# Optimization experiments

Measured on AMD Instinct MI355X. Metric: run time of the kernel, lower is better.

## Reference

```python
import jax, jax.numpy as jnp
import numpy as np

N = 100_000   # nodes
E = 1_600_000 # edges (avg degree 16)
D0, D1, D2 = 128, 64, 64


def _linp(key, n_out, n_in):
    kw, kb = jax.random.split(key)
    s = 1.0 / np.sqrt(n_in)
    W = jax.random.uniform(kw, (n_out, n_in), jnp.float32, -s, s)
    b = jax.random.uniform(kb, (n_out,), jnp.float32, -s, s)
    return W, b


def setup_inputs() -> dict:
    key = jax.random.key(0)
    ks = jax.random.split(key, 9)
    h = jax.random.normal(ks[0], (N, D0), jnp.float32)
    # guarantee every row has at least one edge (avoids empty-row softmax / 0-std NaNs)
    rows = jnp.concatenate([jnp.arange(N, dtype=jnp.int32),
                            jax.random.randint(ks[1], (E - N,), 0, N, jnp.int32)])
    cols = jax.random.randint(ks[2], (E,), 0, N, jnp.int32)
    edge_index = jnp.stack([rows, cols])  # [2, E], row = softmax segment
    W11, b11 = _linp(ks[3], D1, D0)
    W12, b12 = _linp(ks[4], 1, D1)
    W13, b13 = _linp(ks[5], D1, D0)
    W21, b21 = _linp(ks[6], D2, D1)
    W22, b22 = _linp(ks[7], 1, D2)
    W23, b23 = _linp(ks[8], D2, D1)
    return dict(h=h, edge_index=edge_index,
                W11=W11, b11=b11, W12=W12, b12=b12, W13=W13, b13=b13,
                W21=W21, b21=b21, W22=W22, b22=b22, W23=W23, b23=b23)


def reference(h, edge_index, W11, b11, W12, b12, W13, b13,
              W21, b21, W22, b22, W23, b23):
    src, dst = edge_index[0], edge_index[1]

    def gat_layer(x, Wa, ba, We, be, Wv, bv):
        a = jnp.tanh(x @ Wa.T + ba)                       # [N, d] node scores (l11/l21)
        e = jnp.tanh((a[src] + a[dst]) @ We.T + be)[:, 0] # [E] per-edge logit (l12/l22)
        # per-row (segment) softmax over src = row index
        m = jax.ops.segment_max(e, src, num_segments=N)
        ex = jnp.exp(e - m[src])
        denom = jax.ops.segment_sum(ex, src, num_segments=N)
        att = ex / denom[src]                             # [E]
        v = jnp.tanh(x @ Wv.T + bv)                       # [N, d] values (l13/l23)
        out = jax.ops.segment_sum(att[:, None] * v[dst], src, num_segments=N)  # sparse mm
        return out / jnp.std(out, -1, keepdims=True, ddof=1)  # torch.std is unbiased

    h = gat_layer(h, W11, b11, W12, b12, W13, b13)
    h = gat_layer(h, W21, b21, W22, b22, W23, b23)
    return h
```

## Files before the change

kernel.cpp:

```cpp
#include <hip/hip_runtime.h>


#define WS_ALIGN 256
#define BIN_SHIFT 7
#define BIN_NODES 128
#define BIN_CAP 2560
#define MAX_BINS 1024
#define EPB 4096
#define AGGR_BLOCKS 1563

typedef __attribute__((ext_vector_type(8))) short short8;
typedef __attribute__((ext_vector_type(4))) short short4_t;
typedef __attribute__((ext_vector_type(4))) float f32x4;

__device__ __forceinline__ float fast_tanh(float x) {
  x = fminf(15.f, fmaxf(-15.f, x));
  float e = __expf(2.f * x);
  return (e - 1.f) * __builtin_amdgcn_rcpf(e + 1.f);
}

__device__ __forceinline__ unsigned short f32_to_bf16_rne(float f) {
  unsigned u = __float_as_uint(f);
  unsigned r = u + 0x7fffu + ((u >> 16) & 1u);
  return (unsigned short)(r >> 16);
}

__device__ __forceinline__ void prepw_one(const float* __restrict__ Wa,
                                          const float* __restrict__ Wv,
                                          short* __restrict__ Wh, short* __restrict__ Wl,
                                          int K, int i) {
  int KBLK = K / 32;
  int j = i & 7;
  int c = (i >> 3) & 15;
  int q = (i >> 7) & 3;
  int r = i >> 9;
  int nt = r / KBLK, kb = r - nt * KBLK;
  int row = nt * 16 + c;
  int col = kb * 32 + q * 8 + j;
  float f = (row < 64) ? Wa[row * K + col] : Wv[(row - 64) * K + col];
  unsigned u = __float_as_uint(f);
  float hf = __uint_as_float(u & 0xffff0000u);
  Wh[i] = (short)(u >> 16);
  Wl[i] = (short)(__float_as_uint(f - hf) >> 16);
}

__global__ void k_setup(const float* __restrict__ W11, const float* __restrict__ W13,
                        short* __restrict__ Wh1, short* __restrict__ Wl1,
                        const float* __restrict__ W21, const float* __restrict__ W23,
                        short* __restrict__ Wh2, short* __restrict__ Wl2,
                        int* __restrict__ cursor, int nb) {
  int i = blockIdx.x * 256 + threadIdx.x;
  if (i < 16384) {
    prepw_one(W11, W13, Wh1, Wl1, 128, i);
  } else if (i < 16384 + 8192) {
    prepw_one(W21, W23, Wh2, Wl2, 64, i - 16384);
  } else {
    int b = i - 24576;
    if (b < nb) cursor[b] = b * BIN_CAP;
  }
}

__global__ __launch_bounds__(256) void k_bin(const int* __restrict__ src,
                                             const int* __restrict__ dst,
                                             int* __restrict__ cursor,
                                             int* __restrict__ binned, int E, int nb) {
  __shared__ int ssrc[EPB];
  __shared__ int sdst[EPB];
  __shared__ int hist[MAX_BINS];
  __shared__ int base[MAX_BINS];
  int t = threadIdx.x;
  for (int i = t; i < nb; i += 256) hist[i] = 0;
  __syncthreads();
  int e0 = blockIdx.x * EPB;
  for (int i = t; i < EPB; i += 256) {
    int e = e0 + i;
    int sv = -1, dv = 0;
    if (e < E) {
      sv = src[e];
      dv = dst[e];
      atomicAdd(&hist[sv >> BIN_SHIFT], 1);
    }
    ssrc[i] = sv;
    sdst[i] = dv;
  }
  __syncthreads();
  for (int b = t; b < nb; b += 256) {
    int c = hist[b];
    base[b] = c ? atomicAdd(&cursor[b], c) : 0;
    hist[b] = 0;
  }
  __syncthreads();
  for (int i = t; i < EPB; i += 256) {
    int sv = ssrc[i];
    if (sv >= 0) {
      int b = sv >> BIN_SHIFT;
      int r = atomicAdd(&hist[b], 1);
      int pos = base[b] + r;
      if (pos < (b + 1) * BIN_CAP)
        binned[pos] = (sdst[i] << BIN_SHIFT) | (sv & (BIN_NODES - 1));
    }
  }
}

__global__ __launch_bounds__(256) void k_sort_bin(int* __restrict__ binned,
                                                  const int* __restrict__ cursor,
                                                  int* __restrict__ rs,
                                                  int* __restrict__ re, int n) {
  __shared__ int ents[BIN_CAP];
  __shared__ int sorted[BIN_CAP];
  __shared__ int hist[BIN_NODES];
  __shared__ int scan[BIN_NODES];
  __shared__ int cur[BIN_NODES];
  int bin = blockIdx.x;
  int t = threadIdx.x;
  int nbase = bin << BIN_SHIFT;
  int cnt = cursor[bin] - bin * BIN_CAP;
  if (cnt > BIN_CAP) cnt = BIN_CAP;
  if (t < BIN_NODES) hist[t] = 0;
  __syncthreads();
  int* bp = binned + (size_t)bin * BIN_CAP;
  for (int i = t; i < cnt; i += 256) {
    int pk = bp[i];
    ents[i] = pk;
    atomicAdd(&hist[pk & (BIN_NODES - 1)], 1);
  }
  __syncthreads();
  if (t < BIN_NODES) scan[t] = hist[t];
  __syncthreads();
  for (int off = 1; off < BIN_NODES; off <<= 1) {
    int add = (t < BIN_NODES && t >= off) ? scan[t - off] : 0;
    __syncthreads();
    if (t < BIN_NODES) scan[t] += add;
    __syncthreads();
  }
  if (t < BIN_NODES) {
    int ex = scan[t] - hist[t];
    cur[t] = ex;
    int node = nbase + t;
    if (node < n) {
      rs[node] = bin * BIN_CAP + ex;
      re[node] = bin * BIN_CAP + ex + hist[t];
    }
  }
  __syncthreads();
  for (int i = t; i < cnt; i += 256) {
    int pk = ents[i];
    int pos = atomicAdd(&cur[pk & (BIN_NODES - 1)], 1);
    sorted[pos] = pk;
  }
  __syncthreads();
  for (int i = t; i < cnt; i += 256) {
    int pk = sorted[i];
    int node = pk & (BIN_NODES - 1);
    int hi = scan[node];
    int lo = hi - hist[node];
    int r = lo;
    for (int j = lo; j < hi; j++) {
      int pj = sorted[j];
      r += (pj < pk) || (pj == pk && j < i);
    }
    ents[r] = pk >> BIN_SHIFT;
  }
  __syncthreads();
  for (int i = t; i < cnt; i += 256) bp[i] = ents[i];
}

template <int K>
__global__ __launch_bounds__(256) void k_node(
    const float* __restrict__ x, const short* __restrict__ Wh,
    const short* __restrict__ Wl, const float* __restrict__ ba,
    const float* __restrict__ we, const float* __restrict__ bv,
    unsigned short* __restrict__ v_out, float* __restrict__ s_out, int n) {
  constexpr int KBLK = K / 32;
  constexpr int RS = K + 8;
  __shared__ short sah[64 * RS];
  __shared__ short sal[64 * RS];
  __shared__ float sP[2][64];
  int t = threadIdx.x;
  int l = t & 63;
  int w = t >> 6;
  int q = l >> 4, c = l & 15;
  int node0b = blockIdx.x * 64;

  {
    const float4* xg = (const float4*)(x + (size_t)node0b * K);
    constexpr int R4 = K / 4;
#pragma unroll
    for (int it = 0; it < 64 * R4 / 256; it++) {
      int i = it * 256 + t;
      int r = i / R4, k4 = i - r * R4;
      float4 val = (node0b + r < n) ? xg[i] : (float4){0.f, 0.f, 0.f, 0.f};
      float xv[4] = {val.x, val.y, val.z, val.w};
      short4_t hi, lo;
#pragma unroll
      for (int j = 0; j < 4; j++) {
        unsigned u = __float_as_uint(xv[j]);
        hi[j] = (short)(u >> 16);
        float hf = __uint_as_float(u & 0xffff0000u);
        lo[j] = (short)(__float_as_uint(xv[j] - hf) >> 16);
      }
      *(short4_t*)&sah[r * RS + k4 * 4] = hi;
      *(short4_t*)&sal[r * RS + k4 * 4] = lo;
    }
  }

  const short8* WhF = (const short8*)Wh;
  const short8* WlF = (const short8*)Wl;
  short8 wfh[2][KBLK], wfl[2][KBLK];
#pragma unroll
  for (int mt = 0; mt < 2; mt++)
#pragma unroll
    for (int kb = 0; kb < KBLK; kb++) {
      size_t f = (size_t)((2 * w + mt) * KBLK + kb) * 64 + l;
      wfh[mt][kb] = WhF[f];
      wfl[mt][kb] = WlF[f];
    }
  __syncthreads();

  f32x4 acc[4][2];
#pragma unroll
  for (int ns = 0; ns < 4; ns++)
#pragma unroll
    for (int mt = 0; mt < 2; mt++) acc[ns][mt] = (f32x4){0.f, 0.f, 0.f, 0.f};

#pragma unroll
  for (int ns = 0; ns < 4; ns++) {
#pragma unroll
    for (int kb = 0; kb < KBLK; kb++) {
      int off = (ns * 16 + c) * RS + kb * 32 + q * 8;
      short8 ah = *(const short8*)&sah[off];
      short8 al = *(const short8*)&sal[off];
#pragma unroll
      for (int mt = 0; mt < 2; mt++) {
        acc[ns][mt] = __builtin_amdgcn_mfma_f32_16x16x32_bf16(ah, wfh[mt][kb], acc[ns][mt], 0, 0, 0);
        acc[ns][mt] = __builtin_amdgcn_mfma_f32_16x16x32_bf16(ah, wfl[mt][kb], acc[ns][mt], 0, 0, 0);
        acc[ns][mt] = __builtin_amdgcn_mfma_f32_16x16x32_bf16(al, wfh[mt][kb], acc[ns][mt], 0, 0, 0);
      }
    }
  }

  if (w < 2) {
    float bav0 = ba[w * 32 + c], wev0 = we[w * 32 + c];
    float bav1 = ba[w * 32 + 16 + c], wev1 = we[w * 32 + 16 + c];
#pragma unroll
    for (int ns = 0; ns < 4; ns++) {
#pragma unroll
      for (int r = 0; r < 4; r++) {
        float pv = fast_tanh(acc[ns][0][r] + bav0) * wev0 +
                   fast_tanh(acc[ns][1][r] + bav1) * wev1;
#pragma unroll
        for (int mm = 1; mm < 16; mm <<= 1) pv += __shfl_xor(pv, mm, 64);
        if (c == 0) sP[w][ns * 16 + q * 4 + r] = pv;
      }
    }
  } else {
    int wv = w - 2;
    float bvv0 = bv[wv * 32 + c], bvv1 = bv[wv * 32 + 16 + c];
#pragma unroll
    for (int ns = 0; ns < 4; ns++) {
#pragma unroll
      for (int r = 0; r < 4; r++) {
        int node = node0b + ns * 16 + q * 4 + r;
        if (node < n) {
          v_out[(size_t)node * 64 + wv * 32 + c] =
              f32_to_bf16_rne(fast_tanh(acc[ns][0][r] + bvv0));
          v_out[(size_t)node * 64 + wv * 32 + 16 + c] =
              f32_to_bf16_rne(fast_tanh(acc[ns][1][r] + bvv1));
        }
      }
    }
  }
  __syncthreads();
  if (t < 64) {
    int node = node0b + t;
    if (node < n) s_out[node] = sP[0][t] + sP[1][t];
  }
}

__global__ __launch_bounds__(256) void k_aggr(const int* __restrict__ rs,
                                              const int* __restrict__ re,
                                              const int* __restrict__ col,
                                              const float* __restrict__ s,
                                              const float* __restrict__ be_p,
                                              const unsigned short* __restrict__ v,
                                              float* __restrict__ out, int n) {
  int wid = (int)((blockIdx.x * 256 + threadIdx.x) >> 6);
  int nwv = (int)gridDim.x * 4;
  int l = threadIdx.x & 63;
  int q = l >> 4;
  int g = l & 15;
  int qb = l & 48;
  float be = be_p[0];
  int ngroups = (n + 3) >> 2;
  if (wid >= ngroups) return;

  int pnode = wid * 4 + q;
  bool pvn = pnode < n;
  int pe0 = pvn ? rs[pnode] : 0;
  int pe1 = pvn ? re[pnode] : 0;
  float psrow = pvn ? s[pnode] : 0.f;
  int pc;
  float psc;
  {
    int prem = pe1 - pe0;
    pc = (g < prem) ? col[pe0 + g] : 0;
    psc = (g < prem) ? s[pc] : 0.f;
  }

  for (int grp = wid; grp < ngroups; grp += nwv) {
    int e0 = pe0, e1 = pe1;
    float srow = psrow;
    int c0 = pc;
    float sc0 = psc;
    int nxt = grp + nwv;
    if (nxt < ngroups) {
      int nn = nxt * 4 + q;
      bool nv = nn < n;
      pe0 = nv ? rs[nn] : 0;
      pe1 = nv ? re[nn] : 0;
      psrow = nv ? s[nn] : 0.f;
    }
    int m = e1 - e0;
    float a0 = 0.f, a1 = 0.f, a2 = 0.f, a3 = 0.f;
    float dl = 0.f;

    {
      float w = (g < m) ? __expf(fast_tanh(srow + sc0 + be)) : 0.f;
      dl += w;
#pragma unroll
      for (int jj = 0; jj < 16; jj++) {
        int cj = __shfl(c0, qb + jj, 64);
        float wj = __shfl(w, qb + jj, 64);
        uint2 pk = *(const uint2*)(v + ((size_t)cj << 6) + (g << 2));
        a0 = fmaf(wj, __uint_as_float(pk.x << 16), a0);
        a1 = fmaf(wj, __uint_as_float(pk.x & 0xffff0000u), a1);
        a2 = fmaf(wj, __uint_as_float(pk.y << 16), a2);
        a3 = fmaf(wj, __uint_as_float(pk.y & 0xffff0000u), a3);
      }
    }
    if (nxt < ngroups) {
      int nrem = pe1 - pe0;
      pc = (g < nrem) ? col[pe0 + g] : 0;
      psc = (g < nrem) ? s[pc] : 0.f;
    }
    for (int cb = 16; !__all(m - cb <= 0); cb += 16) {
      bool act = (cb + g) < m;
      int c = act ? col[e0 + cb + g] : 0;
      float w = act ? __expf(fast_tanh(srow + s[c] + be)) : 0.f;
      dl += w;
#pragma unroll
      for (int jj = 0; jj < 16; jj++) {
        int cj = __shfl(c, qb + jj, 64);
        float wj = __shfl(w, qb + jj, 64);
        uint2 pk = *(const uint2*)(v + ((size_t)cj << 6) + (g << 2));
        a0 = fmaf(wj, __uint_as_float(pk.x << 16), a0);
        a1 = fmaf(wj, __uint_as_float(pk.x & 0xffff0000u), a1);
        a2 = fmaf(wj, __uint_as_float(pk.y << 16), a2);
        a3 = fmaf(wj, __uint_as_float(pk.y & 0xffff0000u), a3);
      }
    }

#pragma unroll
    for (int mm = 1; mm < 16; mm <<= 1) dl += __shfl_xor(dl, mm, 64);
    float inv = __builtin_amdgcn_rcpf(dl);
    float o0 = a0 * inv, o1 = a1 * inv, o2 = a2 * inv, o3 = a3 * inv;
    float t0 = o0 + o1 + o2 + o3;
    float t1 = o0 * o0 + o1 * o1 + o2 * o2 + o3 * o3;
#pragma unroll
    for (int mm = 1; mm < 16; mm <<= 1) {
      t0 += __shfl_xor(t0, mm, 64);
      t1 += __shfl_xor(t1, mm, 64);
    }
    float var = (t1 - t0 * t0 * (1.0f / 64.f)) * (1.0f / 63.f);
    float isd = __builtin_amdgcn_rsqf(var);
    int cnode = grp * 4 + q;
    if (cnode < n) {
      float4 r = {o0 * isd, o1 * isd, o2 * isd, o3 * isd};
      *(float4*)&out[(size_t)cnode * 64 + (g << 2)] = r;
    }
  }
}

extern "C" void kernel_launch(void* const* d_in, const int* in_sizes, int n_in,
                              void* d_out, int out_size, void* d_ws, size_t ws_size,
                              hipStream_t stream) {
  const float* h = (const float*)d_in[0];
  const int* ei = (const int*)d_in[1];
  const float* W11 = (const float*)d_in[2];
  const float* b11 = (const float*)d_in[3];
  const float* W12 = (const float*)d_in[4];
  const float* b12 = (const float*)d_in[5];
  const float* W13 = (const float*)d_in[6];
  const float* b13 = (const float*)d_in[7];
  const float* W21 = (const float*)d_in[8];
  const float* b21 = (const float*)d_in[9];
  const float* W22 = (const float*)d_in[10];
  const float* b22 = (const float*)d_in[11];
  const float* W23 = (const float*)d_in[12];
  const float* b23 = (const float*)d_in[13];

  const int N = in_sizes[0] / 128;
  const int E = in_sizes[1] / 2;
  const int* src = ei;
  const int* dst = ei + E;
  const int NB = (N + BIN_NODES - 1) >> BIN_SHIFT;

  char* p = (char*)d_ws;
  auto alloc = [&](size_t bytes) -> void* {
    void* r = (void*)p;
    p += (bytes + WS_ALIGN - 1) / WS_ALIGN * WS_ALIGN;
    return r;
  };
  int* cursor = (int*)alloc((size_t)NB * 4);
  int* binned = (int*)alloc((size_t)NB * BIN_CAP * 4);
  int* rsb = (int*)alloc((size_t)N * 4);
  int* reb = (int*)alloc((size_t)N * 4);
  float* sbuf = (float*)alloc((size_t)N * 4);
  unsigned short* vbuf = (unsigned short*)alloc((size_t)N * 64 * 2);
  float* out1 = (float*)alloc((size_t)N * 64 * 4);
  short* Wh1 = (short*)alloc(128 * 128 * 2);
  short* Wl1 = (short*)alloc(128 * 128 * 2);
  short* Wh2 = (short*)alloc(128 * 64 * 2);
  short* Wl2 = (short*)alloc(128 * 64 * 2);

  k_setup<<<(24576 + NB + 255) / 256, 256, 0, stream>>>(
      W11, W13, Wh1, Wl1, W21, W23, Wh2, Wl2, cursor, NB);

  k_bin<<<(E + EPB - 1) / EPB, 256, 0, stream>>>(src, dst, cursor, binned, E, NB);
  k_sort_bin<<<NB, 256, 0, stream>>>(binned, cursor, rsb, reb, N);

  k_node<128><<<(N + 63) / 64, 256, 0, stream>>>(h, Wh1, Wl1, b11, W12, b13, vbuf, sbuf, N);
  k_aggr<<<AGGR_BLOCKS, 256, 0, stream>>>(rsb, reb, binned, sbuf, b12, vbuf, out1, N);

  k_node<64><<<(N + 63) / 64, 256, 0, stream>>>(out1, Wh2, Wl2, b21, W22, b23, vbuf, sbuf, N);
  k_aggr<<<AGGR_BLOCKS, 256, 0, stream>>>(rsb, reb, binned, sbuf, b22, vbuf, (float*)d_out, N);
}
```

Before: 281.6 us.

## Merge setup into binning and run bin sort alongside first node transform

Weight bf16 splitting now runs as extra blocks of the binning kernel, and the cursor init becomes a memset with counts made relative to each bin. The per-bin sort and the first-layer node GEMM are combined into one launch, with blocks choosing their role by block index and sharing a common shared-memory buffer. This cuts kernel launches and lets the independent sort and GEMM work overlap on the device. Aggregation grid size also rises from 1563 to 2048 blocks. The combined kernel reserves the larger of the two shared-memory footprints for every block, which may lower occupancy for the sort blocks.

```diff
diff --git a/kernel.cpp b/kernel.cpp
--- a/kernel.cpp
+++ b/kernel.cpp
@@ -7,7 +7,7 @@
 #define BIN_CAP 2560
 #define MAX_BINS 1024
 #define EPB 4096
-#define AGGR_BLOCKS 1563
+#define AGGR_BLOCKS 2048
 
 typedef __attribute__((ext_vector_type(8))) short short8;
 typedef __attribute__((ext_vector_type(4))) short short4_t;
@@ -44,34 +44,30 @@
   Wl[i] = (short)(__float_as_uint(f - hf) >> 16);
 }
 
-__global__ void k_setup(const float* __restrict__ W11, const float* __restrict__ W13,
-                        short* __restrict__ Wh1, short* __restrict__ Wl1,
-                        const float* __restrict__ W21, const float* __restrict__ W23,
-                        short* __restrict__ Wh2, short* __restrict__ Wl2,
-                        int* __restrict__ cursor, int nb) {
-  int i = blockIdx.x * 256 + threadIdx.x;
-  if (i < 16384) {
-    prepw_one(W11, W13, Wh1, Wl1, 128, i);
-  } else if (i < 16384 + 8192) {
-    prepw_one(W21, W23, Wh2, Wl2, 64, i - 16384);
-  } else {
-    int b = i - 24576;
-    if (b < nb) cursor[b] = b * BIN_CAP;
-  }
-}
-
-__global__ __launch_bounds__(256) void k_bin(const int* __restrict__ src,
-                                             const int* __restrict__ dst,
-                                             int* __restrict__ cursor,
-                                             int* __restrict__ binned, int E, int nb) {
+__global__ __launch_bounds__(256) void k_bin_setup(
+    const int* __restrict__ src, const int* __restrict__ dst,
+    int* __restrict__ cnt0, int* __restrict__ binned, int E, int nb, int binBlks,
+    const float* __restrict__ W11, const float* __restrict__ W13,
+    short* __restrict__ Wh1, short* __restrict__ Wl1,
+    const float* __restrict__ W21, const float* __restrict__ W23,
+    short* __restrict__ Wh2, short* __restrict__ Wl2) {
   __shared__ int ssrc[EPB];
   __shared__ int sdst[EPB];
   __shared__ int hist[MAX_BINS];
   __shared__ int base[MAX_BINS];
   int t = threadIdx.x;
+  if ((int)blockIdx.x >= binBlks) {
+    int i = ((int)blockIdx.x - binBlks) * 256 + t;
+    if (i < 16384) {
+      prepw_one(W11, W13, Wh1, Wl1, 128, i);
+    } else if (i < 24576) {
+      prepw_one(W21, W23, Wh2, Wl2, 64, i - 16384);
+    }
+    return;
+  }
   for (int i = t; i < nb; i += 256) hist[i] = 0;
   __syncthreads();
-  int e0 = blockIdx.x * EPB;
+  int e0 = (int)blockIdx.x * EPB;
   for (int i = t; i < EPB; i += 256) {
     int e = e0 + i;
     int sv = -1, dv = 0;
@@ -86,7 +82,7 @@
   __syncthreads();
   for (int b = t; b < nb; b += 256) {
     int c = hist[b];
-    base[b] = c ? atomicAdd(&cursor[b], c) : 0;
+    base[b] = c ? (b * BIN_CAP + atomicAdd(&cnt0[b], c)) : 0;
     hist[b] = 0;
   }
   __syncthreads();
@@ -102,19 +98,124 @@
   }
 }
 
-__global__ __launch_bounds__(256) void k_sort_bin(int* __restrict__ binned,
-                                                  const int* __restrict__ cursor,
-                                                  int* __restrict__ rs,
-                                                  int* __restrict__ re, int n) {
-  __shared__ int ents[BIN_CAP];
-  __shared__ int sorted[BIN_CAP];
-  __shared__ int hist[BIN_NODES];
-  __shared__ int scan[BIN_NODES];
-  __shared__ int cur[BIN_NODES];
-  int bin = blockIdx.x;
+template <int K>
+__device__ __forceinline__ void node_body(
+    short* __restrict__ sah, short* __restrict__ sal, float* __restrict__ sP,
+    int bid, const float* __restrict__ x, const short* __restrict__ Wh,
+    const short* __restrict__ Wl, const float* __restrict__ ba,
+    const float* __restrict__ we, const float* __restrict__ bv,
+    unsigned short* __restrict__ v_out, float* __restrict__ s_out, int n) {
+  constexpr int KBLK = K / 32;
+  constexpr int RS = K + 8;
+  int t = threadIdx.x;
+  int l = t & 63;
+  int w = t >> 6;
+  int q = l >> 4, c = l & 15;
+  int node0b = bid * 64;
+
+  {
+    const float4* xg = (const float4*)(x + (size_t)node0b * K);
+    constexpr int R4 = K / 4;
+#pragma unroll
+    for (int it = 0; it < 64 * R4 / 256; it++) {
+      int i = it * 256 + t;
+      int r = i / R4, k4 = i - r * R4;
+      float4 val = (node0b + r < n) ? xg[i] : (float4){0.f, 0.f, 0.f, 0.f};
+      float xv[4] = {val.x, val.y, val.z, val.w};
+      short4_t hi, lo;
+#pragma unroll
+      for (int j = 0; j < 4; j++) {
+        unsigned u = __float_as_uint(xv[j]);
+        hi[j] = (short)(u >> 16);
+        float hf = __uint_as_float(u & 0xffff0000u);
+        lo[j] = (short)(__float_as_uint(xv[j] - hf) >> 16);
+      }
+      *(short4_t*)&sah[r * RS + k4 * 4] = hi;
+      *(short4_t*)&sal[r * RS + k4 * 4] = lo;
+    }
+  }
+
+  const short8* WhF = (const short8*)Wh;
+  const short8* WlF = (const short8*)Wl;
+  short8 wfh[2][KBLK], wfl[2][KBLK];
+#pragma unroll
+  for (int mt = 0; mt < 2; mt++)
+#pragma unroll
+    for (int kb = 0; kb < KBLK; kb++) {
+      size_t f = (size_t)((2 * w + mt) * KBLK + kb) * 64 + l;
+      wfh[mt][kb] = WhF[f];
+      wfl[mt][kb] = WlF[f];
+    }
+  __syncthreads();
+
+  f32x4 acc[4][2];
+#pragma unroll
+  for (int ns = 0; ns < 4; ns++)
+#pragma unroll
+    for (int mt = 0; mt < 2; mt++) acc[ns][mt] = (f32x4){0.f, 0.f, 0.f, 0.f};
+
+#pragma unroll
+  for (int ns = 0; ns < 4; ns++) {
+#pragma unroll
+    for (int kb = 0; kb < KBLK; kb++) {
+      int off = (ns * 16 + c) * RS + kb * 32 + q * 8;
+      short8 ah = *(const short8*)&sah[off];
+      short8 al = *(const short8*)&sal[off];
+#pragma unroll
+      for (int mt = 0; mt < 2; mt++) {
+        acc[ns][mt] = __builtin_amdgcn_mfma_f32_16x16x32_bf16(ah, wfh[mt][kb], acc[ns][mt], 0, 0, 0);
+        acc[ns][mt] = __builtin_amdgcn_mfma_f32_16x16x32_bf16(ah, wfl[mt][kb], acc[ns][mt], 0, 0, 0);
+        acc[ns][mt] = __builtin_amdgcn_mfma_f32_16x16x32_bf16(al, wfh[mt][kb], acc[ns][mt], 0, 0, 0);
+      }
+    }
+  }
+
+  if (w < 2) {
+    float bav0 = ba[w * 32 + c], wev0 = we[w * 32 + c];
+    float bav1 = ba[w * 32 + 16 + c], wev1 = we[w * 32 + 16 + c];
+#pragma unroll
+    for (int ns = 0; ns < 4; ns++) {
+#pragma unroll
+      for (int r = 0; r < 4; r++) {
+        float pv = fast_tanh(acc[ns][0][r] + bav0) * wev0 +
+                   fast_tanh(acc[ns][1][r] + bav1) * wev1;
+#pragma unroll
+        for (int mm = 1; mm < 16; mm <<= 1) pv += __shfl_xor(pv, mm, 64);
+        if (c == 0) sP[w * 64 + ns * 16 + q * 4 + r] = pv;
+      }
+    }
+  } else {
+    int wv = w - 2;
+    float bvv0 = bv[wv * 32 + c], bvv1 = bv[wv * 32 + 16 + c];
+#pragma unroll
+    for (int ns = 0; ns < 4; ns++) {
+#pragma unroll
+      for (int r = 0; r < 4; r++) {
+        int node = node0b + ns * 16 + q * 4 + r;
+        if (node < n) {
+          v_out[(size_t)node * 64 + wv * 32 + c] =
+              f32_to_bf16_rne(fast_tanh(acc[ns][0][r] + bvv0));
+          v_out[(size_t)node * 64 + wv * 32 + 16 + c] =
+              f32_to_bf16_rne(fast_tanh(acc[ns][1][r] + bvv1));
+        }
+      }
+    }
+  }
+  __syncthreads();
+  if (t < 64) {
+    int node = node0b + t;
+    if (node < n) s_out[node] = sP[t] + sP[64 + t];
+  }
+}
+
+__device__ __forceinline__ void sort_body(
+    int* __restrict__ ents, int* __restrict__ sorted, int* __restrict__ hist,
+    int* __restrict__ scan, int* __restrict__ cur, int bin,
+    int* __restrict__ binned, const int* __restrict__ cnt0,
+    int* __restrict__ rs, int* __restrict__ re, int n) {
   int t = threadIdx.x;
   int nbase = bin << BIN_SHIFT;
-  int cnt = cursor[bin] - bin * BIN_CAP;
+  int cnt = cnt0[bin];
   if (cnt > BIN_CAP) cnt = BIN_CAP;
   if (t < BIN_NODES) hist[t] = 0;
   __syncthreads();
@@ -165,116 +266,43 @@
   for (int i = t; i < cnt; i += 256) bp[i] = ents[i];
 }
 
+__global__ __launch_bounds__(256) void k_node128_sort(
+    int nodeBlks,
+    const float* __restrict__ x, const short* __restrict__ Wh,
+    const short* __restrict__ Wl, const float* __restrict__ ba,
+    const float* __restrict__ we, const float* __restrict__ bv,
+    unsigned short* __restrict__ v_out, float* __restrict__ s_out, int n,
+    int* __restrict__ binned, const int* __restrict__ cnt0,
+    int* __restrict__ rs, int* __restrict__ re) {
+  __shared__ __align__(16) char smem[64 * 136 * 4 + 512];
+  if ((int)blockIdx.x < nodeBlks) {
+    short* sah = (short*)smem;
+    short* sal = (short*)(smem + 64 * 136 * 2);
+    float* sP = (float*)(smem + 64 * 136 * 4);
+    node_body<128>(sah, sal, sP, (int)blockIdx.x, x, Wh, Wl, ba, we, bv,
+                   v_out, s_out, n);
+  } else {
+    int* ents = (int*)smem;
+    int* sorted = ents + BIN_CAP;
+    int* hist = sorted + BIN_CAP;
+    int* scan = hist + BIN_NODES;
+    int* cur = scan + BIN_NODES;
+    sort_body(ents, sorted, hist, scan, cur, (int)blockIdx.x - nodeBlks,
+              binned, cnt0, rs, re, n);
+  }
+}
+
 template <int K>
 __global__ __launch_bounds__(256) void k_node(
     const float* __restrict__ x, const short* __restrict__ Wh,
     const short* __restrict__ Wl, const float* __restrict__ ba,
     const float* __restrict__ we, const float* __restrict__ bv,
     unsigned short* __restrict__ v_out, float* __restrict__ s_out, int n) {
-  constexpr int KBLK = K / 32;
-  constexpr int RS = K + 8;
-  __shared__ short sah[64 * RS];
-  __shared__ short sal[64 * RS];
-  __shared__ float sP[2][64];
-  int t = threadIdx.x;
-  int l = t & 63;
-  int w = t >> 6;
-  int q = l >> 4, c = l & 15;
-  int node0b = blockIdx.x * 64;
-
-  {
-    const float4* xg = (const float4*)(x + (size_t)node0b * K);
-    constexpr int R4 = K / 4;
-#pragma unroll
-    for (int it = 0; it < 64 * R4 / 256; it++) {
-      int i = it * 256 + t;
-      int r = i / R4, k4 = i - r * R4;
-      float4 val = (node0b + r < n) ? xg[i] : (float4){0.f, 0.f, 0.f, 0.f};
-      float xv[4] = {val.x, val.y, val.z, val.w};
-      short4_t hi, lo;
-#pragma unroll
-      for (int j = 0; j < 4; j++) {
-        unsigned u = __float_as_uint(xv[j]);
-        hi[j] = (short)(u >> 16);
-        float hf = __uint_as_float(u & 0xffff0000u);
-        lo[j] = (short)(__float_as_uint(xv[j] - hf) >> 16);
-      }
-      *(short4_t*)&sah[r * RS + k4 * 4] = hi;
-      *(short4_t*)&sal[r * RS + k4 * 4] = lo;
-    }
-  }
-
-  const short8* WhF = (const short8*)Wh;
-  const short8* WlF = (const short8*)Wl;
-  short8 wfh[2][KBLK], wfl[2][KBLK];
-#pragma unroll
-  for (int mt = 0; mt < 2; mt++)
-#pragma unroll
-    for (int kb = 0; kb < KBLK; kb++) {
-      size_t f = (size_t)((2 * w + mt) * KBLK + kb) * 64 + l;
-      wfh[mt][kb] = WhF[f];
-      wfl[mt][kb] = WlF[f];
-    }
-  __syncthreads();
-
-  f32x4 acc[4][2];
-#pragma unroll
-  for (int ns = 0; ns < 4; ns++)
-#pragma unroll
-    for (int mt = 0; mt < 2; mt++) acc[ns][mt] = (f32x4){0.f, 0.f, 0.f, 0.f};
-
-#pragma unroll
-  for (int ns = 0; ns < 4; ns++) {
-#pragma unroll
-    for (int kb = 0; kb < KBLK; kb++) {
-      int off = (ns * 16 + c) * RS + kb * 32 + q * 8;
-      short8 ah = *(const short8*)&sah[off];
-      short8 al = *(const short8*)&sal[off];
-#pragma unroll
-      for (int mt = 0; mt < 2; mt++) {
-        acc[ns][mt] = __builtin_amdgcn_mfma_f32_16x16x32_bf16(ah, wfh[mt][kb], acc[ns][mt], 0, 0, 0);
-        acc[ns][mt] = __builtin_amdgcn_mfma_f32_16x16x32_bf16(ah, wfl[mt][kb], acc[ns][mt], 0, 0, 0);
-        acc[ns][mt] = __builtin_amdgcn_mfma_f32_16x16x32_bf16(al, wfh[mt][kb], acc[ns][mt], 0, 0, 0);
-      }
-    }
-  }
-
-  if (w < 2) {
-    float bav0 = ba[w * 32 + c], wev0 = we[w * 32 + c];
-    float bav1 = ba[w * 32 + 16 + c], wev1 = we[w * 32 + 16 + c];
-#pragma unroll
-    for (int ns = 0; ns < 4; ns++) {
-#pragma unroll
-      for (int r = 0; r < 4; r++) {
-        float pv = fast_tanh(acc[ns][0][r] + bav0) * wev0 +
-                   fast_tanh(acc[ns][1][r] + bav1) * wev1;
-#pragma unroll
-        for (int mm = 1; mm < 16; mm <<= 1) pv += __shfl_xor(pv, mm, 64);
-        if (c == 0) sP[w][ns * 16 + q * 4 + r] = pv;
-      }
-    }
-  } else {
-    int wv = w - 2;
-    float bvv0 = bv[wv * 32 + c], bvv1 = bv[wv * 32 + 16 + c];
-#pragma unroll
-    for (int ns = 0; ns < 4; ns++) {
-#pragma unroll
-      for (int r = 0; r < 4; r++) {
-        int node = node0b + ns * 16 + q * 4 + r;
-        if (node < n) {
-          v_out[(size_t)node * 64 + wv * 32 + c] =
-              f32_to_bf16_rne(fast_tanh(acc[ns][0][r] + bvv0));
-          v_out[(size_t)node * 64 + wv * 32 + 16 + c] =
-              f32_to_bf16_rne(fast_tanh(acc[ns][1][r] + bvv1));
-        }
-      }
-    }
-  }
-  __syncthreads();
-  if (t < 64) {
-    int node = node0b + t;
-    if (node < n) s_out[node] = sP[0][t] + sP[1][t];
-  }
+  __shared__ short sah[64 * (K + 8)];
+  __shared__ short sal[64 * (K + 8)];
+  __shared__ float sP[2 * 64];
+  node_body<K>(sah, sal, sP, (int)blockIdx.x, x, Wh, Wl, ba, we, bv,
+               v_out, s_out, n);
 }
 
 __global__ __launch_bounds__(256) void k_aggr(const int* __restrict__ rs,
@@ -423,15 +451,21 @@
   short* Wh2 = (short*)alloc(128 * 64 * 2);
   short* Wl2 = (short*)alloc(128 * 64 * 2);
 
-  k_setup<<<(24576 + NB + 255) / 256, 256, 0, stream>>>(
-      W11, W13, Wh1, Wl1, W21, W23, Wh2, Wl2, cursor, NB);
-
-  k_bin<<<(E + EPB - 1) / EPB, 256, 0, stream>>>(src, dst, cursor, binned, E, NB);
-  k_sort_bin<<<NB, 256, 0, stream>>>(binned, cursor, rsb, reb, N);
-
-  k_node<128><<<(N + 63) / 64, 256, 0, stream>>>(h, Wh1, Wl1, b11, W12, b13, vbuf, sbuf, N);
+  const int BIN_BLKS = (E + EPB - 1) / EPB;
+  const int SETUP_BLKS = 24576 / 256;
+  const int NODE_BLKS = (N + 63) / 64;
+
+  (void)hipMemsetAsync(cursor, 0, (size_t)NB * 4, stream);
+  k_bin_setup<<<BIN_BLKS + SETUP_BLKS, 256, 0, stream>>>(
+      src, dst, cursor, binned, E, NB, BIN_BLKS,
+      W11, W13, Wh1, Wl1, W21, W23, Wh2, Wl2);
+
+  k_node128_sort<<<NODE_BLKS + NB, 256, 0, stream>>>(
+      NODE_BLKS, h, Wh1, Wl1, b11, W12, b13, vbuf, sbuf, N,
+      binned, cursor, rsb, reb);
+
   k_aggr<<<AGGR_BLOCKS, 256, 0, stream>>>(rsb, reb, binned, sbuf, b12, vbuf, out1, N);
 
-  k_node<64><<<(N + 63) / 64, 256, 0, stream>>>(out1, Wh2, Wl2, b21, W22, b23, vbuf, sbuf, N);
+  k_node<64><<<NODE_BLKS, 256, 0, stream>>>(out1, Wh2, Wl2, b21, W22, b23, vbuf, sbuf, N);
   k_aggr<<<AGGR_BLOCKS, 256, 0, stream>>>(rsb, reb, binned, sbuf, b22, vbuf, (float*)d_out, N);
 }
```

Result: no change. 277.4 us (-1.5%).
